# Kernel optimization log

Measured on AMD Instinct MI355X. Metric: run time of the kernel, lower is better.

The kernel has to match this reference:

```python
import jax, jax.numpy as jnp
import numpy as np

D_MODEL = 1024
M = 64            # oscillators; state dim N = 2*M
N = 2 * M
N_H = 2           # Householder reflections per step
DT = 0.1
OMEGA_MAX = 100.0
BATCH, SEQ = 8, 2048


def setup_inputs() -> dict:
    key = jax.random.key(0)
    ks = jax.random.split(key, 8)
    u = jax.random.normal(ks[0], (BATCH, SEQ, D_MODEL), jnp.float32)
    # learned parameters (scaled like the module's small-gain init)
    W_A = jax.random.normal(ks[1], (M, D_MODEL), jnp.float32) * 0.01
    b_A = jnp.zeros((M,), jnp.float32)
    W_k = jax.random.normal(ks[2], (N_H, N, D_MODEL), jnp.float32) * 0.02
    b_k = jnp.zeros((N_H, N), jnp.float32)
    W_beta = jax.random.normal(ks[3], (N_H, D_MODEL), jnp.float32) * 0.02
    b_beta = jnp.zeros((N_H,), jnp.float32)
    B_w = jax.random.normal(ks[4], (N, D_MODEL), jnp.float32) * 0.02
    B_b = jnp.zeros((N,), jnp.float32)
    C = jax.random.normal(ks[5], (D_MODEL, N), jnp.float32) * 0.01
    D = jax.random.normal(ks[6], (D_MODEL,), jnp.float32) * 0.01
    return dict(u=u, W_A=W_A, b_A=b_A, W_k=W_k, b_k=b_k,
                W_beta=W_beta, b_beta=b_beta, B_w=B_w, B_b=B_b, C=C, D=D)


def reference(u, W_A, b_A, W_k, b_k, W_beta, b_beta, B_w, B_b, C, D):
    batch = u.shape[0]
    # --- precompute all input-dependent per-step quantities as big GEMMs ---
    A = jax.nn.relu(jnp.einsum('btd,md->btm', u, W_A) + b_A)
    A = jnp.minimum(A, OMEGA_MAX)                       # clamp(max=omega_max)
    S = 1.0 / (1.0 + (DT * DT) * A)                     # (B,T,M)
    K = jnp.einsum('btd,jnd->btjn', u, W_k) + b_k       # (B,T,n_h,N)
    K = K / jnp.maximum(jnp.linalg.norm(K, axis=-1, keepdims=True), 1e-12)
    beta = 2.0 * jax.nn.sigmoid(jnp.einsum('btd,jd->btj', u, W_beta) + b_beta)
    Bt = jnp.einsum('btd,nd->btn', u, B_w) + B_b        # (B,T,N)

    # time-major for scan
    xs = (jnp.moveaxis(A, 1, 0), jnp.moveaxis(S, 1, 0), jnp.moveaxis(K, 1, 0),
          jnp.moveaxis(beta, 1, 0), jnp.moveaxis(Bt, 1, 0))
    h0 = jnp.zeros((batch, N), u.dtype)

    def step(h, x):
        A_t, S_t, K_t, beta_t, B_t = x
        # oscillatory rotation-contraction R_t @ h (m 2x2 blocks)
        z, y = h[:, :M], h[:, M:]
        z_new = S_t * z - DT * A_t * S_t * y
        y_new = DT * S_t * z + S_t * y
        h = jnp.concatenate([z_new, y_new], axis=-1)
        # sequential Householder product H_t @ h (fixed small n_h loop)
        for j in range(N_H):
            k = K_t[:, j]                                # (B,N), unit norm
            dot = jnp.sum(k * h, axis=-1, keepdims=True)
            h = h - beta_t[:, j:j + 1] * k * dot
        h = h + B_t
        return h, h

    _, hs = jax.lax.scan(step, h0, xs)                  # (T,B,N)
    hs = jnp.moveaxis(hs, 0, 1)                         # (B,T,N)
    return jnp.einsum('btn,dn->btd', hs, C) + u * D
```

## Files before the change

kernel.cpp:

```cpp
#include <hip/hip_runtime.h>
#include <cmath>


#define NTOK 16384
#define TT 2048
#define BB 8
#define DM 1024
#define FS 520
#define CH 32
#define LCH 64
#define NW 448
#define NWP 512

typedef short bf16x8 __attribute__((ext_vector_type(8)));
typedef float f32x4 __attribute__((ext_vector_type(4)));

#define GLOAD_LDS16(g, l)                                          \
  __builtin_amdgcn_global_load_lds(                                \
      (const __attribute__((address_space(1))) void*)(g),          \
      (__attribute__((address_space(3))) void*)(l), 16, 0, 0)

__global__ __launch_bounds__(256) void packW(
    const float* __restrict__ W_A, const float* __restrict__ b_A,
    const float* __restrict__ W_k, const float* __restrict__ b_k,
    const float* __restrict__ b_beta,
    const float* __restrict__ B_w, const float* __restrict__ B_b,
    float* __restrict__ Wp, float* __restrict__ bias) {
  int r = blockIdx.x;
  int tid = threadIdx.x;
  const float* src;
  float bv;
  if (r < 64)       { src = W_A + (size_t)r * DM;         bv = b_A[r]; }
  else if (r < 320) { src = W_k + (size_t)(r - 64) * DM;  bv = b_k[r - 64]; }
  else              { src = B_w + (size_t)(r - 320) * DM; bv = B_b[r - 320]; }
  ((float4*)(Wp + (size_t)r * DM))[tid] = ((const float4*)src)[tid];
  if (tid == 0) bias[r] = bv;
  if (r == 0 && tid < 2) bias[448 + tid] = b_beta[tid];
}

__global__ __launch_bounds__(256) void transK(
    const float* __restrict__ src, float* __restrict__ dst, int M, int N) {
  __shared__ float tile[64][68];
  const int m0 = blockIdx.x * 64, n0 = blockIdx.y * 64;
  const int tid = threadIdx.x;
#pragma unroll
  for (int l = 0; l < 4; ++l) {
    int idx = tid + l * 256;
    int r = idx >> 4, c4 = (idx & 15) * 4;
    float4 v = *(const float4*)(src + (size_t)(m0 + r) * N + n0 + c4);
    tile[r][c4 + 0] = v.x; tile[r][c4 + 1] = v.y;
    tile[r][c4 + 2] = v.z; tile[r][c4 + 3] = v.w;
  }
  __syncthreads();
#pragma unroll
  for (int l = 0; l < 4; ++l) {
    int idx = tid + l * 256;
    int c = idx >> 4, r4 = (idx & 15) * 4;
    float4 w = make_float4(tile[r4 + 0][c], tile[r4 + 1][c],
                           tile[r4 + 2][c], tile[r4 + 3][c]);
    *(float4*)(dst + (size_t)(n0 + c) * M + m0 + r4) = w;
  }
}

__device__ inline unsigned short bf16_rne(float x) {
  unsigned b = __float_as_uint(x);
  b += 0x7FFFu + ((b >> 16) & 1u);
  return (unsigned short)(b >> 16);
}

__device__ inline void split_bf16(float x, unsigned short& h, unsigned short& l) {
  unsigned b = __float_as_uint(x);
  h = (unsigned short)(b >> 16);
  float rem = x - __uint_as_float(b & 0xFFFF0000u);
  l = bf16_rne(rem);
}

__global__ __launch_bounds__(256) void convertU(
    const float* __restrict__ u, unsigned short* __restrict__ uh,
    unsigned short* __restrict__ ul) {
  int gid = blockIdx.x * 256 + threadIdx.x;
  int m = gid >> 8;
  int g = gid & 255;
  float4 v = *(const float4*)(u + (size_t)m * DM + g * 4);
  int kt = g >> 3, gg = g & 7;
  int p = gg & 3, h = gg >> 2;
  int mr = m & 127, mb = m >> 7;
  int pp = p ^ ((mr >> 2) & 3);
  size_t dst = ((size_t)(mb * 32 + kt)) * 4096 + mr * 32 + ((pp << 1) | h) * 4;
  ushort4 hi, lo;
  split_bf16(v.x, hi.x, lo.x);
  split_bf16(v.y, hi.y, lo.y);
  split_bf16(v.z, hi.z, lo.z);
  split_bf16(v.w, hi.w, lo.w);
  *(ushort4*)(uh + dst) = hi;
  *(ushort4*)(ul + dst) = lo;
}

__global__ __launch_bounds__(256) void convertW(
    const float* __restrict__ Wp, unsigned short* __restrict__ Wb) {
  int gid = blockIdx.x * 256 + threadIdx.x;
  int n = gid >> 8, g = gid & 255;
  int kt = g >> 3, gg = g & 7;
  int p = gg & 3, h = gg >> 2;
  int nr = n & 127, nb = n >> 7;
  int pp = p ^ ((nr >> 2) & 3);
  size_t dst = ((size_t)(nb * 32 + kt)) * 4096 + nr * 32 + ((pp << 1) | h) * 4;
  ushort4 hv = make_ushort4(0, 0, 0, 0);
  if (n < NW) {
    float4 v = *(const float4*)(Wp + (size_t)n * DM + g * 4);
    hv.x = bf16_rne(v.x); hv.y = bf16_rne(v.y);
    hv.z = bf16_rne(v.z); hv.w = bf16_rne(v.w);
  }
  *(ushort4*)(Wb + dst) = hv;
}

__global__ __launch_bounds__(256) void gemmA_mfma(
    const unsigned short* __restrict__ uh, const unsigned short* __restrict__ ul,
    const unsigned short* __restrict__ Wb, float* __restrict__ Feat, int npass) {
  __shared__ __align__(16) unsigned short As[4096];
  __shared__ __align__(16) unsigned short Bs[4096];
  const int tid = threadIdx.x;
  const int wv = tid >> 6, ln = tid & 63;
  const int lr = ln & 15, G = ln >> 4;
  const int wm = wv >> 1, wn = wv & 1;
  const int x = G ^ (lr >> 2);
  f32x4 acc[4][4];
#pragma unroll
  for (int i = 0; i < 4; ++i)
#pragma unroll
    for (int j = 0; j < 4; ++j) acc[i][j] = (f32x4){0.f, 0.f, 0.f, 0.f};

  const size_t aBase = (size_t)blockIdx.x * 32 * 4096;
  const size_t bBase = (size_t)blockIdx.y * 32 * 4096;
  const int so = wv * 512 + ln * 8;
  const int ld = wv * 512;

  for (int pass = 0; pass < npass; ++pass) {
    const unsigned short* ua = pass ? ul : uh;
    for (int kt = 0; kt < 32; ++kt) {
      const unsigned short* ga = ua + aBase + (size_t)kt * 4096;
      const unsigned short* gb = Wb + bBase + (size_t)kt * 4096;
      GLOAD_LDS16(ga + so,        As + ld);
      GLOAD_LDS16(ga + 2048 + so, As + 2048 + ld);
      GLOAD_LDS16(gb + so,        Bs + ld);
      GLOAD_LDS16(gb + 2048 + so, Bs + 2048 + ld);
      __syncthreads();
      bf16x8 af[4], bfr[4];
      const char* Ab = (const char*)As + ((wm * 64 + lr) << 6) + (x << 4);
      const char* Bb = (const char*)Bs + ((wn * 64 + lr) << 6) + (x << 4);
#pragma unroll
      for (int i = 0; i < 4; ++i) {
        af[i]  = *(const bf16x8*)(Ab + i * 1024);
        bfr[i] = *(const bf16x8*)(Bb + i * 1024);
      }
#pragma unroll
      for (int i = 0; i < 4; ++i)
#pragma unroll
        for (int j = 0; j < 4; ++j)
          acc[i][j] = __builtin_amdgcn_mfma_f32_16x16x32_bf16(
              af[i], bfr[j], acc[i][j], 0, 0, 0);
      __syncthreads();
    }
  }
  const int row0 = (blockIdx.x << 7) + wm * 64 + (G << 2);
  const int col0 = (blockIdx.y << 7) + wn * 64 + lr;
  float* fb = Feat + (size_t)row0 * FS + col0;
#pragma unroll
  for (int i = 0; i < 4; ++i)
#pragma unroll
    for (int j = 0; j < 4; ++j) {
      float* d = fb + (size_t)(i * 16) * FS + j * 16;
#pragma unroll
      for (int r = 0; r < 4; ++r) d[(size_t)r * FS] = acc[i][j][r];
    }
}

__global__ __launch_bounds__(256) void gemmA_f32(
    const float* __restrict__ u, const float* __restrict__ WpT,
    float* __restrict__ Feat) {
  __shared__ float us2[128][36];
  __shared__ float wsm[32][68];
  const int tid = threadIdx.x;
  const int tx = tid & 15, ty = tid >> 4;
  const int m0 = blockIdx.x * 128;
  const int n0 = blockIdx.y * 64;
  float acc[8][4];
#pragma unroll
  for (int i = 0; i < 8; ++i)
#pragma unroll
    for (int j = 0; j < 4; ++j) acc[i][j] = 0.f;

  for (int k0 = 0; k0 < DM; k0 += 32) {
#pragma unroll
    for (int l = 0; l < 4; ++l) {
      int idx = tid + l * 256;
      int r = idx >> 3, c4 = (idx & 7) * 4;
      float4 v = *(const float4*)(u + (size_t)(m0 + r) * DM + k0 + c4);
      *(float4*)&us2[r][c4] = v;
    }
#pragma unroll
    for (int l = 0; l < 2; ++l) {
      int idx = tid + l * 256;
      int k = idx >> 4, c4 = (idx & 15) * 4;
      float4 v = *(const float4*)(WpT + (size_t)(k0 + k) * NW + n0 + c4);
      *(float4*)&wsm[k][c4] = v;
    }
    __syncthreads();
#pragma unroll
    for (int k4 = 0; k4 < 8; ++k4) {
      float4 bq0 = *(const float4*)&wsm[4 * k4 + 0][tx * 4];
      float4 bq1 = *(const float4*)&wsm[4 * k4 + 1][tx * 4];
      float4 bq2 = *(const float4*)&wsm[4 * k4 + 2][tx * 4];
      float4 bq3 = *(const float4*)&wsm[4 * k4 + 3][tx * 4];
#pragma unroll
      for (int i = 0; i < 8; ++i) {
        float4 a = *(const float4*)&us2[ty * 8 + i][4 * k4];
        acc[i][0] = fmaf(a.x, bq0.x, acc[i][0]);
        acc[i][1] = fmaf(a.x, bq0.y, acc[i][1]);
        acc[i][2] = fmaf(a.x, bq0.z, acc[i][2]);
        acc[i][3] = fmaf(a.x, bq0.w, acc[i][3]);
        acc[i][0] = fmaf(a.y, bq1.x, acc[i][0]);
        acc[i][1] = fmaf(a.y, bq1.y, acc[i][1]);
        acc[i][2] = fmaf(a.y, bq1.z, acc[i][2]);
        acc[i][3] = fmaf(a.y, bq1.w, acc[i][3]);
        acc[i][0] = fmaf(a.z, bq2.x, acc[i][0]);
        acc[i][1] = fmaf(a.z, bq2.y, acc[i][1]);
        acc[i][2] = fmaf(a.z, bq2.z, acc[i][2]);
        acc[i][3] = fmaf(a.z, bq2.w, acc[i][3]);
        acc[i][0] = fmaf(a.w, bq3.x, acc[i][0]);
        acc[i][1] = fmaf(a.w, bq3.y, acc[i][1]);
        acc[i][2] = fmaf(a.w, bq3.z, acc[i][2]);
        acc[i][3] = fmaf(a.w, bq3.w, acc[i][3]);
      }
    }
    __syncthreads();
  }
#pragma unroll
  for (int i = 0; i < 8; ++i) {
    float4 v = make_float4(acc[i][0], acc[i][1], acc[i][2], acc[i][3]);
    *(float4*)(Feat + (size_t)(m0 + ty * 8 + i) * FS + n0 + tx * 4) = v;
  }
}

__device__ inline float wave_sum(float v) {
#pragma unroll
  for (int off = 32; off > 0; off >>= 1) v += __shfl_xor(v, off, 64);
  return v;
}

__global__ __launch_bounds__(64) void postA(float* __restrict__ Feat,
                                            const float* __restrict__ bias,
                                            const float* __restrict__ u,
                                            const float* __restrict__ Wb) {
  const int t = blockIdx.x, lane = threadIdx.x;
  float* f = Feat + (size_t)t * FS;
  float s0 = 0.f, s1 = 0.f;
#pragma unroll
  for (int j = 0; j < 4; ++j) {
    float4 uv = *(const float4*)(u + (size_t)t * DM + j * 256 + lane * 4);
    float4 w0 = *(const float4*)(Wb + j * 256 + lane * 4);
    float4 w1 = *(const float4*)(Wb + DM + j * 256 + lane * 4);
    s0 = fmaf(uv.x, w0.x, s0); s0 = fmaf(uv.y, w0.y, s0);
    s0 = fmaf(uv.z, w0.z, s0); s0 = fmaf(uv.w, w0.w, s0);
    s1 = fmaf(uv.x, w1.x, s1); s1 = fmaf(uv.y, w1.y, s1);
    s1 = fmaf(uv.z, w1.z, s1); s1 = fmaf(uv.w, w1.w, s1);
  }
  s0 = wave_sum(s0); s1 = wave_sum(s1);
  float a = f[lane] + bias[lane];
  a = fminf(fmaxf(a, 0.f), 100.f);
  float S = 1.f / (1.f + 0.01f * a);
  f[lane] = S;
  f[448 + lane] = 0.1f * a * S;
  float k10 = f[64 + lane] + bias[64 + lane];
  float k11 = f[128 + lane] + bias[128 + lane];
  float n1 = wave_sum(k10 * k10 + k11 * k11);
  float inv1 = 1.f / fmaxf(sqrtf(n1), 1e-12f);
  k10 *= inv1; k11 *= inv1;
  f[64 + lane] = k10; f[128 + lane] = k11;
  float k20 = f[192 + lane] + bias[192 + lane];
  float k21 = f[256 + lane] + bias[256 + lane];
  float n2 = wave_sum(k20 * k20 + k21 * k21);
  float inv2 = 1.f / fmaxf(sqrtf(n2), 1e-12f);
  k20 *= inv2; k21 *= inv2;
  f[192 + lane] = k20; f[256 + lane] = k21;
  float c12 = wave_sum(k10 * k20 + k11 * k21);
  if (lane == 0) {
    f[512] = 2.f / (1.f + expf(-(s0 + bias[448])));
    f[513] = 2.f / (1.f + expf(-(s1 + bias[449])));
    f[514] = c12;
  }
  f[320 + lane] += bias[320 + lane];
  f[384 + lane] += bias[384 + lane];
}

__global__ __launch_bounds__(512, 2) void scanB1(
    const float* __restrict__ Feat, float* __restrict__ Mc) {
  const int cid = blockIdx.x;
  const int t0 = (cid >> 5) * TT + (cid & 31) * LCH;
  const int tid = threadIdx.x;
  const int col = tid >> 2, q = tid & 3;
  const int i0 = q * 16;
  __shared__ float fb[2][4 * FS];
  float mz[16], my[16];
#pragma unroll
  for (int j = 0; j < 16; ++j) {
    mz[j] = (i0 + j == col) ? 1.f : 0.f;
    my[j] = (64 + i0 + j == col) ? 1.f : 0.f;
  }
  {
    const float4* src = (const float4*)(Feat + (size_t)t0 * FS);
    for (int v = tid; v < FS; v += 512) ((float4*)fb[0])[v] = src[v];
  }
  __syncthreads();
  for (int g = 0; g < 16; ++g) {
    const int cur = g & 1;
    float4 pf0, pf1;
    const bool has2 = tid < (FS - 512);
    if (g < 15) {
      const float4* src = (const float4*)(Feat + (size_t)(t0 + (g + 1) * 4) * FS);
      pf0 = src[tid];
      if (has2) pf1 = src[tid + 512];
    }
#pragma unroll
    for (int s = 0; s < 4; ++s) {
      const float* f = fb[cur] + s * FS;
      float sj[16], cj[16], k1z[16], k1y[16], k2z[16], k2y[16];
#pragma unroll
      for (int v = 0; v < 4; ++v) {
        *(float4*)&sj[4 * v]  = *(const float4*)(f + i0 + 4 * v);
        *(float4*)&cj[4 * v]  = *(const float4*)(f + 448 + i0 + 4 * v);
        *(float4*)&k1z[4 * v] = *(const float4*)(f + 64 + i0 + 4 * v);
        *(float4*)&k1y[4 * v] = *(const float4*)(f + 128 + i0 + 4 * v);
        *(float4*)&k2z[4 * v] = *(const float4*)(f + 192 + i0 + 4 * v);
        *(float4*)&k2y[4 * v] = *(const float4*)(f + 256 + i0 + 4 * v);
      }
      float4 sc = *(const float4*)(f + 512);
      float p = 0.f, r2 = 0.f;
#pragma unroll
      for (int j = 0; j < 16; ++j) {
        float s0 = sj[j], c1 = cj[j];
        float z = mz[j], y = my[j];
        float sz = s0 * z;
        z = fmaf(-c1, y, sz);
        y = fmaf(s0, y, 0.1f * sz);
        mz[j] = z; my[j] = y;
        p  = fmaf(k1z[j], z, p);  p  = fmaf(k1y[j], y, p);
        r2 = fmaf(k2z[j], z, r2); r2 = fmaf(k2y[j], y, r2);
      }
      p  += __shfl_xor(p, 1, 64);  p  += __shfl_xor(p, 2, 64);
      r2 += __shfl_xor(r2, 1, 64); r2 += __shfl_xor(r2, 2, 64);
      float e1 = sc.x * p;
      float e2 = sc.y * fmaf(-sc.z, e1, r2);
#pragma unroll
      for (int j = 0; j < 16; ++j) {
        float z = fmaf(-e1, k1z[j], mz[j]);
        mz[j] = fmaf(-e2, k2z[j], z);
        float y = fmaf(-e1, k1y[j], my[j]);
        my[j] = fmaf(-e2, k2y[j], y);
      }
    }
    if (g < 15) {
      ((float4*)fb[1 - cur])[tid] = pf0;
      if (has2) ((float4*)fb[1 - cur])[tid + 512] = pf1;
    }
    __syncthreads();
  }
  float* dst = Mc + ((size_t)cid * 128 + col) * 128;
#pragma unroll
  for (int v = 0; v < 4; ++v)
    *(float4*)(dst + i0 + 4 * v) = *(float4*)&mz[4 * v];
#pragma unroll
  for (int v = 0; v < 4; ++v)
    *(float4*)(dst + 64 + i0 + 4 * v) = *(float4*)&my[4 * v];
}

__global__ __launch_bounds__(64) void scanB0(
    const float* __restrict__ Feat, float* __restrict__ dc) {
  const int cid = blockIdx.x;
  const int lane = threadIdx.x;
  float z = 0.f, y = 0.f;
  const int t0 = (cid >> 5) * TT + (cid & 31) * LCH;
  for (int t = t0; t < t0 + LCH; ++t) {
    const float* __restrict__ f = Feat + (size_t)t * FS;
    float s = f[lane], c1 = f[448 + lane];
    float k1z = f[64 + lane], k1y = f[128 + lane];
    float k2z = f[192 + lane], k2y = f[256 + lane];
    float bz = f[320 + lane], by = f[384 + lane];
    float b1 = f[512], b2 = f[513], c12 = f[514];
    float sz = s * z;
    float zn = fmaf(-c1, y, sz);
    float yn = fmaf(s, y, 0.1f * sz);
    float p = fmaf(k1y, yn, k1z * zn);
    float qq = fmaf(k2y, yn, k2z * zn);
#pragma unroll
    for (int off = 32; off > 0; off >>= 1) {
      p += __shfl_xor(p, off, 64);
      qq += __shfl_xor(qq, off, 64);
    }
    float e1 = b1 * p;
    float d2 = fmaf(-c12, e1, qq);
    float e2 = b2 * d2;
    z = fmaf(-e1, k1z, zn); z = fmaf(-e2, k2z, z); z += bz;
    y = fmaf(-e1, k1y, yn); y = fmaf(-e2, k2y, y); y += by;
  }
  dc[(size_t)cid * 128 + lane] = z;
  dc[(size_t)cid * 128 + 64 + lane] = y;
}

__global__ __launch_bounds__(256) void scanB2(
    const float* __restrict__ Mc, const float* __restrict__ dc,
    float* __restrict__ hstart) {
  const int b = blockIdx.x;
  const int tid = threadIdx.x;
  const int i = tid & 127, jh = tid >> 7;
  __shared__ float h[128];
  __shared__ float red[2][128];
  if (tid < 128) h[tid] = 0.f;
  __syncthreads();
  float mreg[64];
  {
    const float* M0 = Mc + (size_t)(b * CH) * 16384;
#pragma unroll
    for (int j = 0; j < 64; ++j) mreg[j] = M0[(size_t)(jh * 64 + j) * 128 + i];
  }
  for (int c = 0; c < CH; ++c) {
    if (tid < 128) hstart[(size_t)(b * CH + c) * 128 + tid] = h[tid];
    float acc = 0.f;
#pragma unroll
    for (int j = 0; j < 64; ++j) acc = fmaf(mreg[j], h[jh * 64 + j], acc);
    red[jh][i] = acc;
    if (c + 1 < CH) {
      const float* Mn = Mc + (size_t)(b * CH + c + 1) * 16384;
#pragma unroll
      for (int j = 0; j < 64; ++j) mreg[j] = Mn[(size_t)(jh * 64 + j) * 128 + i];
    }
    __syncthreads();
    if (tid < 128)
      h[tid] = red[0][tid] + red[1][tid] + dc[(size_t)(b * CH + c) * 128 + tid];
    __syncthreads();
  }
}

__global__ __launch_bounds__(64) void scanB3(
    const float* __restrict__ Feat, const float* __restrict__ hstart,
    float* __restrict__ hs) {
  const int cid = blockIdx.x;
  const int lane = threadIdx.x;
  float z = hstart[(size_t)cid * 128 + lane];
  float y = hstart[(size_t)cid * 128 + 64 + lane];
  const int t0 = (cid >> 5) * TT + (cid & 31) * LCH;
  for (int t = t0; t < t0 + LCH; ++t) {
    const float* __restrict__ f = Feat + (size_t)t * FS;
    float s = f[lane], c1 = f[448 + lane];
    float k1z = f[64 + lane], k1y = f[128 + lane];
    float k2z = f[192 + lane], k2y = f[256 + lane];
    float bz = f[320 + lane], by = f[384 + lane];
    float b1 = f[512], b2 = f[513], c12 = f[514];
    float sz = s * z;
    float zn = fmaf(-c1, y, sz);
    float yn = fmaf(s, y, 0.1f * sz);
    float p = fmaf(k1y, yn, k1z * zn);
    float qq = fmaf(k2y, yn, k2z * zn);
#pragma unroll
    for (int off = 32; off > 0; off >>= 1) {
      p += __shfl_xor(p, off, 64);
      qq += __shfl_xor(qq, off, 64);
    }
    float e1 = b1 * p;
    float d2 = fmaf(-c12, e1, qq);
    float e2 = b2 * d2;
    zn = fmaf(-e1, k1z, zn); zn = fmaf(-e2, k2z, zn); zn += bz;
    yn = fmaf(-e1, k1y, yn); yn = fmaf(-e2, k2y, yn); yn += by;
    hs[(size_t)t * 128 + lane] = zn;
    hs[(size_t)t * 128 + 64 + lane] = yn;
    z = zn; y = yn;
  }
}

__global__ __launch_bounds__(256) void gemmC(
    const float* __restrict__ hs, const float* __restrict__ CmT,
    const float* __restrict__ u, const float* __restrict__ Dv,
    float* __restrict__ out) {
  __shared__ float as2[64][68];
  __shared__ float bs[64][68];
  const int tid = threadIdx.x;
  const int tx = tid & 15, ty = tid >> 4;
  const int t0 = blockIdx.x * 64;
  const int d0 = blockIdx.y * 64;
  float acc[4][4];
#pragma unroll
  for (int i = 0; i < 4; ++i)
#pragma unroll
    for (int j = 0; j < 4; ++j) acc[i][j] = 0.f;

  for (int kb = 0; kb < 128; kb += 64) {
#pragma unroll
    for (int l = 0; l < 4; ++l) {
      int idx = tid + l * 256;
      int r = idx >> 4, c4 = (idx & 15) * 4;
      float4 v = *(const float4*)(hs + (size_t)(t0 + r) * 128 + kb + c4);
      *(float4*)&as2[r][c4] = v;
      float4 w = *(const float4*)(CmT + (size_t)(kb + r) * DM + d0 + c4);
      *(float4*)&bs[r][c4] = w;
    }
    __syncthreads();
#pragma unroll
    for (int k4 = 0; k4 < 16; ++k4) {
      float4 bq0 = *(const float4*)&bs[4 * k4 + 0][tx * 4];
      float4 bq1 = *(const float4*)&bs[4 * k4 + 1][tx * 4];
      float4 bq2 = *(const float4*)&bs[4 * k4 + 2][tx * 4];
      float4 bq3 = *(const float4*)&bs[4 * k4 + 3][tx * 4];
#pragma unroll
      for (int i = 0; i < 4; ++i) {
        float4 a = *(const float4*)&as2[ty * 4 + i][4 * k4];
        acc[i][0] = fmaf(a.x, bq0.x, acc[i][0]);
        acc[i][1] = fmaf(a.x, bq0.y, acc[i][1]);
        acc[i][2] = fmaf(a.x, bq0.z, acc[i][2]);
        acc[i][3] = fmaf(a.x, bq0.w, acc[i][3]);
        acc[i][0] = fmaf(a.y, bq1.x, acc[i][0]);
        acc[i][1] = fmaf(a.y, bq1.y, acc[i][1]);
        acc[i][2] = fmaf(a.y, bq1.z, acc[i][2]);
        acc[i][3] = fmaf(a.y, bq1.w, acc[i][3]);
        acc[i][0] = fmaf(a.z, bq2.x, acc[i][0]);
        acc[i][1] = fmaf(a.z, bq2.y, acc[i][1]);
        acc[i][2] = fmaf(a.z, bq2.z, acc[i][2]);
        acc[i][3] = fmaf(a.z, bq2.w, acc[i][3]);
        acc[i][0] = fmaf(a.w, bq3.x, acc[i][0]);
        acc[i][1] = fmaf(a.w, bq3.y, acc[i][1]);
        acc[i][2] = fmaf(a.w, bq3.z, acc[i][2]);
        acc[i][3] = fmaf(a.w, bq3.w, acc[i][3]);
      }
    }
    __syncthreads();
  }
#pragma unroll
  for (int i = 0; i < 4; ++i) {
    int row = t0 + ty * 4 + i;
    float4 uv = *(const float4*)(u + (size_t)row * DM + d0 + tx * 4);
    float4 dv = *(const float4*)(Dv + d0 + tx * 4);
    float4 o;
    o.x = fmaf(uv.x, dv.x, acc[i][0]);
    o.y = fmaf(uv.y, dv.y, acc[i][1]);
    o.z = fmaf(uv.z, dv.z, acc[i][2]);
    o.w = fmaf(uv.w, dv.w, acc[i][3]);
    *(float4*)(out + (size_t)row * DM + d0 + tx * 4) = o;
  }
}

extern "C" void kernel_launch(void* const* d_in, const int* in_sizes, int n_in,
                              void* d_out, int out_size, void* d_ws, size_t ws_size,
                              hipStream_t stream) {
  const float* u      = (const float*)d_in[0];
  const float* W_A    = (const float*)d_in[1];
  const float* b_A    = (const float*)d_in[2];
  const float* W_k    = (const float*)d_in[3];
  const float* b_k    = (const float*)d_in[4];
  const float* W_beta = (const float*)d_in[5];
  const float* b_beta = (const float*)d_in[6];
  const float* B_w    = (const float*)d_in[7];
  const float* B_b    = (const float*)d_in[8];
  const float* Cm     = (const float*)d_in[9];
  const float* Dv     = (const float*)d_in[10];
  float* out = (float*)d_out;
  char* ws = (char*)d_ws;
  float* Wp     = (float*)(ws);
  float* WpT    = (float*)(ws + 1835008);
  unsigned short* Wb = (unsigned short*)(ws + 1835008);
  float* CmT    = (float*)(ws + 3670016);
  float* bias   = (float*)(ws + 4194304);
  float* Feat   = (float*)(ws + 4198400);
  float* Mc     = (float*)(ws + 38277120);
  float* dcv    = (float*)(ws + 55054336);
  float* hstart = (float*)(ws + 55185408);
  float* hsb    = (float*)(ws + 55316480);
  unsigned short* uh = (unsigned short*)(ws + 38277120);
  unsigned short* ul = (unsigned short*)(ws + 71831552);
  const size_t NEED1 = 71831552 + 0;
  const size_t NEED2 = 105385984;

  packW<<<dim3(448), dim3(256), 0, stream>>>(W_A, b_A, W_k, b_k, b_beta,
                                             B_w, B_b, Wp, bias);
  transK<<<dim3(16, 2), dim3(256), 0, stream>>>(Cm, CmT, DM, 128);

  const bool big1 = (ws_size == 0) || (ws_size >= NEED1);
  const bool big2 = (ws_size == 0) || (ws_size >= NEED2);
  if (big1) {
    const int npass = big2 ? 2 : 1;
    convertW<<<dim3(512), dim3(256), 0, stream>>>(Wp, Wb);
    convertU<<<dim3(16384), dim3(256), 0, stream>>>(u, uh, big2 ? ul : uh);
    gemmA_mfma<<<dim3(128, 4), dim3(256), 0, stream>>>(uh, ul, Wb, Feat, npass);
  } else {
    transK<<<dim3(7, 16), dim3(256), 0, stream>>>(Wp, WpT, NW, DM);
    gemmA_f32<<<dim3(128, 7), dim3(256), 0, stream>>>(u, WpT, Feat);
  }
  postA<<<dim3(16384), dim3(64), 0, stream>>>(Feat, bias, u, W_beta);
  scanB1<<<dim3(256), dim3(512), 0, stream>>>(Feat, Mc);
  scanB0<<<dim3(256), dim3(64), 0, stream>>>(Feat, dcv);
  scanB2<<<dim3(8), dim3(256), 0, stream>>>(Mc, dcv, hstart);
  scanB3<<<dim3(256), dim3(64), 0, stream>>>(Feat, hstart, hsb);
  gemmC<<<dim3(256, 16), dim3(256), 0, stream>>>(hsb, CmT, u, Dv, out);
}
```

Measured before the change: 437.3 us.

## Run output projection GEMM on MFMA with split-bf16 three-pass precision

Result: faster. 423.3 us (-3.2%).

```diff
diff --git a/kernel.cpp b/kernel.cpp
--- a/kernel.cpp
+++ b/kernel.cpp
@@ -114,6 +114,27 @@
   *(ushort4*)(Wb + dst) = hv;
 }
 
+__global__ __launch_bounds__(256) void convertC(
+    const float* __restrict__ Cm, unsigned short* __restrict__ Chp,
+    unsigned short* __restrict__ Clp) {
+  int gid = blockIdx.x * 256 + threadIdx.x;
+  int d = gid >> 5;
+  int g = gid & 31;
+  float4 v = *(const float4*)(Cm + (size_t)d * 128 + g * 4);
+  int kt = g >> 3, gg = g & 7;
+  int p = gg & 3, h = gg >> 2;
+  int nr = d & 127, nb = d >> 7;
+  int pp = p ^ ((nr >> 2) & 3);
+  size_t dst = ((size_t)(nb * 4 + kt)) * 4096 + nr * 32 + ((pp << 1) | h) * 4;
+  ushort4 hi, lo;
+  split_bf16(v.x, hi.x, lo.x);
+  split_bf16(v.y, hi.y, lo.y);
+  split_bf16(v.z, hi.z, lo.z);
+  split_bf16(v.w, hi.w, lo.w);
+  *(ushort4*)(Chp + dst) = hi;
+  *(ushort4*)(Clp + dst) = lo;
+}
+
 __global__ __launch_bounds__(256) void gemmA_mfma(
     const unsigned short* __restrict__ uh, const unsigned short* __restrict__ ul,
     const unsigned short* __restrict__ Wb, float* __restrict__ Feat, int npass) {
@@ -173,6 +194,75 @@
 #pragma unroll
       for (int r = 0; r < 4; ++r) d[(size_t)r * FS] = acc[i][j][r];
     }
+}
+
+__global__ __launch_bounds__(256) void gemmC_mfma(
+    const unsigned short* __restrict__ hsh, const unsigned short* __restrict__ hsl,
+    const unsigned short* __restrict__ Chp, const unsigned short* __restrict__ Clp,
+    const float* __restrict__ u, const float* __restrict__ Dv,
+    float* __restrict__ out) {
+  __shared__ __align__(16) unsigned short As[4096];
+  __shared__ __align__(16) unsigned short Bs[4096];
+  const int tid = threadIdx.x;
+  const int wv = tid >> 6, ln = tid & 63;
+  const int lr = ln & 15, G = ln >> 4;
+  const int wm = wv >> 1, wn = wv & 1;
+  const int x = G ^ (lr >> 2);
+  f32x4 acc[4][4];
+#pragma unroll
+  for (int i = 0; i < 4; ++i)
+#pragma unroll
+    for (int j = 0; j < 4; ++j) acc[i][j] = (f32x4){0.f, 0.f, 0.f, 0.f};
+
+  const size_t aBase = (size_t)blockIdx.x * 4 * 4096;
+  const size_t bBase = (size_t)blockIdx.y * 4 * 4096;
+  const int so = wv * 512 + ln * 8;
+  const int ld = wv * 512;
+
+#pragma unroll 1
+  for (int pass = 0; pass < 3; ++pass) {
+    const unsigned short* pa = (pass == 1) ? hsl : hsh;
+    const unsigned short* pb = (pass == 2) ? Clp : Chp;
+#pragma unroll 1
+    for (int kt = 0; kt < 4; ++kt) {
+      const unsigned short* ga = pa + aBase + (size_t)kt * 4096;
+      const unsigned short* gb = pb + bBase + (size_t)kt * 4096;
+      GLOAD_LDS16(ga + so,        As + ld);
+      GLOAD_LDS16(ga + 2048 + so, As + 2048 + ld);
+      GLOAD_LDS16(gb + so,        Bs + ld);
+      GLOAD_LDS16(gb + 2048 + so, Bs + 2048 + ld);
+      __syncthreads();
+      bf16x8 af[4], bfr[4];
+      const char* Ab = (const char*)As + ((wm * 64 + lr) << 6) + (x << 4);
+      const char* Bb = (const char*)Bs + ((wn * 64 + lr) << 6) + (x << 4);
+#pragma unroll
+      for (int i = 0; i < 4; ++i) {
+        af[i]  = *(const bf16x8*)(Ab + i * 1024);
+        bfr[i] = *(const bf16x8*)(Bb + i * 1024);
+      }
+#pragma unroll
+      for (int i = 0; i < 4; ++i)
+#pragma unroll
+        for (int j = 0; j < 4; ++j)
+          acc[i][j] = __builtin_amdgcn_mfma_f32_16x16x32_bf16(
+              af[i], bfr[j], acc[i][j], 0, 0, 0);
+      __syncthreads();
+    }
+  }
+  const int row0 = (blockIdx.x << 7) + wm * 64 + (G << 2);
+  const int col0 = (blockIdx.y << 7) + wn * 64 + lr;
+#pragma unroll
+  for (int j = 0; j < 4; ++j) {
+    float dv = Dv[col0 + j * 16];
+#pragma unroll
+    for (int i = 0; i < 4; ++i) {
+#pragma unroll
+      for (int r = 0; r < 4; ++r) {
+        size_t off = (size_t)(row0 + i * 16 + r) * DM + col0 + j * 16;
+        out[off] = fmaf(u[off], dv, acc[i][j][r]);
+      }
+    }
+  }
 }
 
 __global__ __launch_bounds__(256) void gemmA_f32(
@@ -443,12 +533,17 @@
 
 __global__ __launch_bounds__(64) void scanB3(
     const float* __restrict__ Feat, const float* __restrict__ hstart,
-    float* __restrict__ hs) {
+    float* __restrict__ hs, unsigned short* __restrict__ hsh,
+    unsigned short* __restrict__ hsl, int split) {
   const int cid = blockIdx.x;
   const int lane = threadIdx.x;
   float z = hstart[(size_t)cid * 128 + lane];
   float y = hstart[(size_t)cid * 128 + 64 + lane];
   const int t0 = (cid >> 5) * TT + (cid & 31) * LCH;
+  const int ktz = lane >> 5, kkz = lane & 31;
+  const int kty = (64 + lane) >> 5, kky = lane & 31;
+  const int pz = (kkz >> 2) & 3, hz = kkz >> 4;
+  const int lowz = kkz & 3;
   for (int t = t0; t < t0 + LCH; ++t) {
     const float* __restrict__ f = Feat + (size_t)t * FS;
     float s = f[lane], c1 = f[448 + lane];
@@ -471,10 +566,30 @@
     float e2 = b2 * d2;
     zn = fmaf(-e1, k1z, zn); zn = fmaf(-e2, k2z, zn); zn += bz;
     yn = fmaf(-e1, k1y, yn); yn = fmaf(-e2, k2y, yn); yn += by;
-    hs[(size_t)t * 128 + lane] = zn;
-    hs[(size_t)t * 128 + 64 + lane] = yn;
+    if (split) {
+      const int mb = t >> 7, mr = t & 127;
+      const int xr = (mr >> 2) & 3;
+      {
+        size_t idx = ((size_t)(mb * 4 + ktz)) * 4096 + mr * 32 +
+                     ((((pz ^ xr) << 1) | hz)) * 4 + lowz;
+        unsigned short hi, lo;
+        split_bf16(zn, hi, lo);
+        hsh[idx] = hi; hsl[idx] = lo;
+      }
+      {
+        size_t idx = ((size_t)(mb * 4 + kty)) * 4096 + mr * 32 +
+                     ((((pz ^ xr) << 1) | hz)) * 4 + lowz;
+        unsigned short hi, lo;
+        split_bf16(yn, hi, lo);
+        hsh[idx] = hi; hsl[idx] = lo;
+      }
+    } else {
+      hs[(size_t)t * 128 + lane] = zn;
+      hs[(size_t)t * 128 + 64 + lane] = yn;
+    }
     z = zn; y = yn;
   }
+  (void)kky;
 }
 
 __global__ __launch_bounds__(256) void gemmC(
@@ -575,7 +690,11 @@
   float* hsb    = (float*)(ws + 55316480);
   unsigned short* uh = (unsigned short*)(ws + 38277120);
   unsigned short* ul = (unsigned short*)(ws + 71831552);
-  const size_t NEED1 = 71831552 + 0;
+  unsigned short* hsh = (unsigned short*)(ws + 71831552);
+  unsigned short* hsl = (unsigned short*)(ws + 76025856);
+  unsigned short* Chp = (unsigned short*)(ws + 80220160);
+  unsigned short* Clp = (unsigned short*)(ws + 80482304);
+  const size_t NEED1 = 71831552;
   const size_t NEED2 = 105385984;
 
   packW<<<dim3(448), dim3(256), 0, stream>>>(W_A, b_A, W_k, b_k, b_beta,
@@ -589,6 +708,8 @@
     convertW<<<dim3(512), dim3(256), 0, stream>>>(Wp, Wb);
     convertU<<<dim3(16384), dim3(256), 0, stream>>>(u, uh, big2 ? ul : uh);
     gemmA_mfma<<<dim3(128, 4), dim3(256), 0, stream>>>(uh, ul, Wb, Feat, npass);
+    if (big2)
+      convertC<<<dim3(128), dim3(256), 0, stream>>>(Cm, Chp, Clp);
   } else {
     transK<<<dim3(7, 16), dim3(256), 0, stream>>>(Wp, WpT, NW, DM);
     gemmA_f32<<<dim3(128, 7), dim3(256), 0, stream>>>(u, WpT, Feat);
@@ -597,6 +718,12 @@
   scanB1<<<dim3(256), dim3(512), 0, stream>>>(Feat, Mc);
   scanB0<<<dim3(256), dim3(64), 0, stream>>>(Feat, dcv);
   scanB2<<<dim3(8), dim3(256), 0, stream>>>(Mc, dcv, hstart);
-  scanB3<<<dim3(256), dim3(64), 0, stream>>>(Feat, hstart, hsb);
-  gemmC<<<dim3(256, 16), dim3(256), 0, stream>>>(hsb, CmT, u, Dv, out);
-}
+  if (big2) {
+    scanB3<<<dim3(256), dim3(64), 0, stream>>>(Feat, hstart, hsb, hsh, hsl, 1);
+    gemmC_mfma<<<dim3(128, 8), dim3(256), 0, stream>>>(hsh, hsl, Chp, Clp,
+                                                       u, Dv, out);
+  } else {
+    scanB3<<<dim3(256), dim3(64), 0, stream>>>(Feat, hstart, hsb, hsh, hsl, 0);
+    gemmC<<<dim3(256, 16), dim3(256), 0, stream>>>(hsb, CmT, u, Dv, out);
+  }
+}
```
